# Kernel tuning notes

Measured on AMD Instinct MI355X. Metric: run time of the kernel, lower is better.

The kernel has to match this reference:

```python
import jax, jax.numpy as jnp
import numpy as np

DIM = 768
HEADS = 12
HEAD_DIM = DIM // HEADS
EPS = 1e-5


def setup_inputs() -> dict:
    key = jax.random.key(0)
    ks = jax.random.split(key, 9)
    s = 0.02
    x = jax.random.normal(ks[0], (4, 1024, DIM), dtype=jnp.float32)
    return {
        "x": x,
        "Wqkv_c": jax.random.normal(ks[1], (DIM, 3 * DIM), jnp.float32) * s,
        "bqkv_c": jnp.zeros((3 * DIM,), jnp.float32),
        "Wp_c": jax.random.normal(ks[2], (DIM, DIM), jnp.float32) * s,
        "bp_c": jnp.zeros((DIM,), jnp.float32),
        "Wqkv_ac": jax.random.normal(ks[3], (DIM, 3 * DIM), jnp.float32) * s,
        "bqkv_ac": jnp.zeros((3 * DIM,), jnp.float32),
        "Wp_ac": jax.random.normal(ks[4], (DIM, DIM), jnp.float32) * s,
        "bp_ac": jnp.zeros((DIM,), jnp.float32),
        "gamma": jnp.ones((DIM,), jnp.float32),
        "beta": jnp.zeros((DIM,), jnp.float32),
    }


def _branch(x, Wqkv, bqkv, Wp, bp, causal: bool):
    B, T, C = x.shape
    qkv = (x @ Wqkv + bqkv).reshape(B, T, 3, HEADS, HEAD_DIM)
    qkv = jnp.transpose(qkv, (2, 0, 3, 1, 4))  # [3,B,H,T,Dh]
    q, k, v = qkv[0], qkv[1], qkv[2]
    scores = jnp.einsum("bhqd,bhkd->bhqk", q, k) / np.sqrt(HEAD_DIM).astype(np.float32)
    i = jnp.arange(T)[:, None]
    j = jnp.arange(T)[None, :]
    mask = (j <= i) if causal else (j >= i)  # tril / triu (incl. diagonal)
    scores = jnp.where(mask[None, None], scores, -jnp.inf)
    attn = jax.nn.softmax(scores, axis=-1)
    out = jnp.einsum("bhqk,bhkd->bhqd", attn, v)
    out = jnp.transpose(out, (0, 2, 1, 3)).reshape(B, T, C)
    return out @ Wp + bp


def reference(x, Wqkv_c, bqkv_c, Wp_c, bp_c, Wqkv_ac, bqkv_ac, Wp_ac, bp_ac, gamma, beta):
    out_c = _branch(x, Wqkv_c, bqkv_c, Wp_c, bp_c, causal=True)
    out_ac = _branch(x, Wqkv_ac, bqkv_ac, Wp_ac, bp_ac, causal=False)
    y = x + out_c + out_ac  # residual; dropout is identity at eval
    mu = jnp.mean(y, axis=-1, keepdims=True)
    var = jnp.var(y, axis=-1, keepdims=True)
    return (y - mu) * jax.lax.rsqrt(var + EPS) * gamma + beta
```

## Files before the change

### kernel.cpp

```cpp
#include <hip/hip_runtime.h>
#include <stdint.h>

#define DIM 768
#define HEADS 12
#define HD 64
#define BATCH 4
#define SEQ 1024
#define NTOK (BATCH*SEQ)
#define QKVW (3*DIM)
#define QKW (2*DIM)
#define EPS 1e-5f

typedef __attribute__((ext_vector_type(8))) short short8;
typedef __attribute__((ext_vector_type(4))) float f32x4;

__device__ __forceinline__ unsigned short f2bf(float f) {
    union { float f; unsigned u; } v; v.f = f;
    unsigned r = v.u + 0x7fffu + ((v.u >> 16) & 1u);
    return (unsigned short)(r >> 16);
}
__device__ __forceinline__ float b2f(unsigned short s) {
    union { unsigned u; float f; } v; v.u = (unsigned)s << 16; return v.f;
}

__device__ __forceinline__ void gld_lds16(const void* g, void* l) {
    auto gp = reinterpret_cast<const __attribute__((address_space(1))) unsigned int*>(
        (uintptr_t)g);
    auto lp = reinterpret_cast<__attribute__((address_space(3))) unsigned int*>(
        (unsigned int)(uintptr_t)l);
    __builtin_amdgcn_global_load_lds(gp, lp, 16, 0, 0);
}

#define CVT_X_BLOCKS (NTOK*DIM/4096)
#define CVT_WQ_TILES ((QKVW/32)*(DIM/32))
#define CVT_WP_TILES ((DIM/32)*(DIM/32))
__global__ __launch_bounds__(256) void cvt_all_kernel(
    const float* __restrict__ x,
    const float* __restrict__ Wq0, const float* __restrict__ Wq1,
    const float* __restrict__ Wp0, const float* __restrict__ Wp1,
    unsigned short* __restrict__ xb,
    unsigned short* __restrict__ WqT0, unsigned short* __restrict__ WqT1,
    unsigned short* __restrict__ WpT0, unsigned short* __restrict__ WpT1)
{
    const int bid = blockIdx.x, tid = threadIdx.x;
    if (bid < CVT_X_BLOCKS) {
        const int base = bid * 1024 + tid;
#pragma unroll
        for (int u = 0; u < 4; ++u) {
            const float4 v = ((const float4*)x)[base + u * 256];
            ushort4 o4;
            o4.x = f2bf(v.x); o4.y = f2bf(v.y); o4.z = f2bf(v.z); o4.w = f2bf(v.w);
            ((ushort4*)xb)[base + u * 256] = o4;
        }
        return;
    }
    __shared__ float t[32][33];
    const float* W; unsigned short* WT; int N, K, tile;
    int w = bid - CVT_X_BLOCKS;
    if (w < 2 * CVT_WQ_TILES) {
        const int z = w / CVT_WQ_TILES; tile = w % CVT_WQ_TILES;
        W = z ? Wq1 : Wq0; WT = z ? WqT1 : WqT0; N = QKVW; K = DIM;
    } else {
        w -= 2 * CVT_WQ_TILES;
        const int z = w / CVT_WP_TILES; tile = w % CVT_WP_TILES;
        W = z ? Wp1 : Wp0; WT = z ? WpT1 : WpT0; N = DIM; K = DIM;
    }
    const int ntiles = N / 32;
    const int n0 = (tile % ntiles) * 32, k0 = (tile / ntiles) * 32;
    const int c = tid & 31, rr = tid >> 5;
#pragma unroll
    for (int i = 0; i < 4; ++i)
        t[rr + 8 * i][c] = W[(size_t)(k0 + rr + 8 * i) * N + n0 + c];
    __syncthreads();
#pragma unroll
    for (int i = 0; i < 4; ++i)
        WT[(size_t)(n0 + rr + 8 * i) * K + k0 + c] = f2bf(t[c][rr + 8 * i]);
}

__global__ __launch_bounds__(256) void gemm_qkv_kernel(
    const unsigned short* __restrict__ A,
    const unsigned short* __restrict__ BT0, const unsigned short* __restrict__ BT1,
    const float* __restrict__ bias0, const float* __restrict__ bias1,
    unsigned short* __restrict__ QK0, unsigned short* __restrict__ QK1,
    unsigned short* __restrict__ VT0, unsigned short* __restrict__ VT1)
{
    const int gid = blockIdx.x;
    const int g = gid & 7, t = gid >> 3;
    const int bx = (g & 1) * 9 + t % 9;
    const int by = ((g >> 1) & 1) * 16 + t / 9;
    const int z = g >> 2;
    const unsigned short* __restrict__ BT = z ? BT1 : BT0;
    const float* __restrict__ bias = z ? bias1 : bias0;
    unsigned short* __restrict__ QK = z ? QK1 : QK0;
    unsigned short* __restrict__ VT = z ? VT1 : VT0;
    const int K = DIM;
    const int m0 = by * 128, n0 = bx * 128;

    __shared__ __align__(16) unsigned short sh[17408];
    const int tid = threadIdx.x, lane = tid & 63, wv = tid >> 6;
    const int wr = wv >> 1, wc = wv & 1;
    const int fm = lane & 15, fk = (lane >> 4) * 8;
    const int c0 = wv * 2;
    const int arow = c0 * 16 + (lane >> 2), kk = (lane & 3) * 8;

    const unsigned short* Ag0 = A  + (size_t)(m0 + arow)      * K + kk;
    const unsigned short* Ag1 = A  + (size_t)(m0 + arow + 16) * K + kk;
    const unsigned short* Bg0 = BT + (size_t)(n0 + arow)      * K + kk;
    const unsigned short* Bg1 = BT + (size_t)(n0 + arow + 16) * K + kk;

    f32x4 acc[4][4];
#pragma unroll
    for (int i = 0; i < 4; ++i)
#pragma unroll
        for (int j = 0; j < 4; ++j) acc[i][j] = f32x4{0.f, 0.f, 0.f, 0.f};

    gld_lds16(Ag0, &sh[c0 * 512]);
    gld_lds16(Ag1, &sh[c0 * 512 + 512]);
    gld_lds16(Bg0, &sh[4096 + c0 * 512]);
    gld_lds16(Bg1, &sh[4096 + c0 * 512 + 512]);

    const int NK = K / 32;
    for (int kt = 0; kt < NK; ++kt) {
        const int p = kt & 1;
        __syncthreads();
        if (kt + 1 < NK) {
            const int off = (kt + 1) * 32;
            const int q = (p ^ 1) * 8192;
            gld_lds16(Ag0 + off, &sh[q + c0 * 512]);
            gld_lds16(Ag1 + off, &sh[q + c0 * 512 + 512]);
            gld_lds16(Bg0 + off, &sh[q + 4096 + c0 * 512]);
            gld_lds16(Bg1 + off, &sh[q + 4096 + c0 * 512 + 512]);
        }
        const int pb = p * 8192;
        short8 af[4], bf[4];
#pragma unroll
        for (int i = 0; i < 4; ++i)
            af[i] = *(const short8*)&sh[pb + (wr * 64 + i * 16 + fm) * 32 + fk];
#pragma unroll
        for (int j = 0; j < 4; ++j)
            bf[j] = *(const short8*)&sh[pb + 4096 + (wc * 64 + j * 16 + fm) * 32 + fk];
#pragma unroll
        for (int i = 0; i < 4; ++i)
#pragma unroll
            for (int j = 0; j < 4; ++j)
                acc[i][j] = __builtin_amdgcn_mfma_f32_16x16x32_bf16(af[i], bf[j], acc[i][j], 0, 0, 0);
    }

    __syncthreads();
    const int rbase = (lane >> 4) * 4;
    const int rowg = tid >> 4, lseg = tid & 15;
    if (n0 < QKW) {
        const float qsc = (n0 < DIM) ? 0.125f : 1.0f;
#pragma unroll
        for (int i = 0; i < 4; ++i) {
            const int ml = wr * 64 + i * 16 + rbase;
#pragma unroll
            for (int j = 0; j < 4; ++j) {
                const int nl = wc * 64 + j * 16 + fm;
                const float bs = bias[n0 + nl];
#pragma unroll
                for (int r = 0; r < 4; ++r)
                    sh[(ml + r) * 136 + nl] = f2bf((acc[i][j][r] + bs) * qsc);
            }
        }
        __syncthreads();
#pragma unroll
        for (int pp = 0; pp < 8; ++pp) {
            const int row = pp * 16 + rowg;
            const uint4 v = *(const uint4*)&sh[row * 136 + lseg * 8];
            *(uint4*)(QK + (size_t)(m0 + row) * QKW + n0 + lseg * 8) = v;
        }
    } else {
        const int b = m0 >> 10, t0 = m0 & 1023;
#pragma unroll
        for (int i = 0; i < 4; ++i) {
            const int tl = wr * 64 + i * 16 + rbase;
#pragma unroll
            for (int j = 0; j < 4; ++j) {
                const int nl = wc * 64 + j * 16 + fm;
                const float bs = bias[n0 + nl];
                const unsigned p0 = f2bf(acc[i][j][0] + bs);
                const unsigned p1 = f2bf(acc[i][j][1] + bs);
                const unsigned p2 = f2bf(acc[i][j][2] + bs);
                const unsigned p3 = f2bf(acc[i][j][3] + bs);
                uint2 u; u.x = p0 | (p1 << 16); u.y = p2 | (p3 << 16);
                *(uint2*)(&sh[nl * 136 + tl]) = u;
            }
        }
        __syncthreads();
#pragma unroll
        for (int pp = 0; pp < 8; ++pp) {
            const int nl = pp * 16 + rowg;
            const int nh = (n0 - QKW) + nl;
            const uint4 v = *(const uint4*)&sh[nl * 136 + lseg * 8];
            *(uint4*)(VT + ((size_t)((b * HEADS + (nh >> 6)) * HD + (nh & 63))) * SEQ
                      + t0 + lseg * 8) = v;
        }
    }
}

__global__ __launch_bounds__(256) void gemm_proj_kernel(
    const unsigned short* __restrict__ A0, const unsigned short* __restrict__ BT0,
    const unsigned short* __restrict__ A1, const unsigned short* __restrict__ BT1,
    const float* __restrict__ b0, const float* __restrict__ b1,
    const float* __restrict__ xres, float* __restrict__ Y0,
    unsigned short* __restrict__ Y1)
{
    const int z = blockIdx.z;
    const unsigned short* __restrict__ A  = z ? A1 : A0;
    const unsigned short* __restrict__ BT = z ? BT1 : BT0;
    __shared__ __align__(16) unsigned short Als[2][64 * 32];
    __shared__ __align__(16) unsigned short Bls[2][128 * 32];
    const int tid = threadIdx.x, lane = tid & 63, wv = tid >> 6;
    const int m0 = blockIdx.y * 64, n0 = blockIdx.x * 128;
    const int fm = lane & 15, fg = lane >> 4, fk = (lane >> 4) * 8;
    const int srw = lane >> 2, kk = (lane & 3) * 8;
    const int K = DIM;

    const unsigned short* Ag  = A  + (size_t)(m0 + wv * 16 + srw) * K + kk;
    const unsigned short* Bg0 = BT + (size_t)(n0 + wv * 32 + srw) * K + kk;
    const unsigned short* Bg1 = BT + (size_t)(n0 + wv * 32 + 16 + srw) * K + kk;

    f32x4 acc[4][2];
#pragma unroll
    for (int i = 0; i < 4; ++i)
#pragma unroll
        for (int j = 0; j < 2; ++j) acc[i][j] = f32x4{0.f, 0.f, 0.f, 0.f};

    gld_lds16(Ag,  &Als[0][wv * 512]);
    gld_lds16(Bg0, &Bls[0][wv * 1024]);
    gld_lds16(Bg1, &Bls[0][wv * 1024 + 512]);

    const int NK = K / 32;
    for (int kt = 0; kt < NK; ++kt) {
        const int p = kt & 1;
        __syncthreads();
        if (kt + 1 < NK) {
            const int off = (kt + 1) * 32;
            gld_lds16(Ag + off,  &Als[p ^ 1][wv * 512]);
            gld_lds16(Bg0 + off, &Bls[p ^ 1][wv * 1024]);
            gld_lds16(Bg1 + off, &Bls[p ^ 1][wv * 1024 + 512]);
        }
        short8 af[4], bf[2];
#pragma unroll
        for (int i = 0; i < 4; ++i)
            af[i] = *(const short8*)&Als[p][(i * 16 + fm) * 32 + fk];
#pragma unroll
        for (int j = 0; j < 2; ++j)
            bf[j] = *(const short8*)&Bls[p][(wv * 32 + j * 16 + fm) * 32 + fk];
#pragma unroll
        for (int i = 0; i < 4; ++i)
#pragma unroll
            for (int j = 0; j < 2; ++j)
                acc[i][j] = __builtin_amdgcn_mfma_f32_16x16x32_bf16(af[i], bf[j], acc[i][j], 0, 0, 0);
    }
#pragma unroll
    for (int i = 0; i < 4; ++i) {
        const int m = m0 + i * 16 + fg * 4;
#pragma unroll
        for (int j = 0; j < 2; ++j) {
            const int n = n0 + wv * 32 + j * 16 + fm;
            if (z == 0) {
                const float bs = b0[n] + b1[n];
#pragma unroll
                for (int r = 0; r < 4; ++r) {
                    const size_t idx = (size_t)(m + r) * DIM + n;
                    Y0[idx] = acc[i][j][r] + xres[idx] + bs;
                }
            } else {
#pragma unroll
                for (int r = 0; r < 4; ++r)
                    Y1[(size_t)(m + r) * DIM + n] = f2bf(acc[i][j][r]);
            }
        }
    }
}

#define KP 72
__global__ __launch_bounds__(256, 3) void attn_fused_kernel(
    const unsigned short* __restrict__ qk_c, const unsigned short* __restrict__ vT_c,
    const unsigned short* __restrict__ qk_ac, const unsigned short* __restrict__ vT_ac,
    unsigned short* __restrict__ o_c, unsigned short* __restrict__ o_ac)
{
    __shared__ __align__(16) unsigned short Kls[2][64 * KP];
    __shared__ __align__(16) unsigned short Vls[2][64 * KP];
    __shared__ __align__(16) unsigned short Ps[4][16 * KP];
    const int tid = threadIdx.x, lane = tid & 63, w = tid >> 6;
    const int fm = lane & 15, fg = lane >> 4;
    const int bh = blockIdx.x, qt = blockIdx.y;
    const int b = bh / HEADS, h = bh % HEADS;
    unsigned short* Psw = &Ps[w][0];
    const int srow = tid >> 3, sseg = (tid & 7) * 8;

    for (int br = 0; br < 2; ++br) {
        const int causal = (br == 0);
        const unsigned short* __restrict__ qk = causal ? qk_c : qk_ac;
        const unsigned short* __restrict__ vT = causal ? vT_c : vT_ac;
        unsigned short* __restrict__ o = causal ? o_c : o_ac;
        const unsigned short* qbase = qk + (size_t)b * SEQ * QKW + h * HD;
        const unsigned short* kbase = qbase + DIM;
        const unsigned short* vtb   = vT + (size_t)(b * HEADS + h) * HD * SEQ;

        short8 qb0, qb1;
        {
            const size_t qoff = (size_t)(qt * 64 + w * 16 + fm) * QKW + fg * 8;
            qb0 = *(const short8*)(qbase + qoff);
            qb1 = *(const short8*)(qbase + qoff + 32);
        }

        float ls = 0.f;
        f32x4 accO[4];
#pragma unroll
        for (int dj = 0; dj < 4; ++dj) accO[dj] = f32x4{0.f, 0.f, 0.f, 0.f};

        const int ktb = causal ? 0 : qt;
        const int kte = causal ? qt : (SEQ / 64 - 1);

        uint4 kr0 = *(const uint4*)(kbase + (size_t)(ktb * 64 + srow) * QKW + sseg);
        uint4 kr1 = *(const uint4*)(kbase + (size_t)(ktb * 64 + srow + 32) * QKW + sseg);
        uint4 vr0 = *(const uint4*)(vtb + (size_t)srow * SEQ + ktb * 64 + sseg);
        uint4 vr1 = *(const uint4*)(vtb + (size_t)(srow + 32) * SEQ + ktb * 64 + sseg);

        if (br) __syncthreads();
        int p = 0;
        for (int kt = ktb; kt <= kte; ++kt) {
            *(uint4*)(&Kls[p][srow * KP + sseg])        = kr0;
            *(uint4*)(&Kls[p][(srow + 32) * KP + sseg]) = kr1;
            *(uint4*)(&Vls[p][srow * KP + sseg])        = vr0;
            *(uint4*)(&Vls[p][(srow + 32) * KP + sseg]) = vr1;
            if (kt < kte) {
                const int ktn = kt + 1;
                kr0 = *(const uint4*)(kbase + (size_t)(ktn * 64 + srow) * QKW + sseg);
                kr1 = *(const uint4*)(kbase + (size_t)(ktn * 64 + srow + 32) * QKW + sseg);
                vr0 = *(const uint4*)(vtb + (size_t)srow * SEQ + ktn * 64 + sseg);
                vr1 = *(const uint4*)(vtb + (size_t)(srow + 32) * SEQ + ktn * 64 + sseg);
            }
            __syncthreads();

            f32x4 st[4];
#pragma unroll
            for (int kj = 0; kj < 4; ++kj) {
                const short8 ka0 = *(const short8*)&Kls[p][(kj * 16 + fm) * KP + fg * 8];
                const short8 ka1 = *(const short8*)&Kls[p][(kj * 16 + fm) * KP + 32 + fg * 8];
                st[kj] = __builtin_amdgcn_mfma_f32_16x16x32_bf16(ka0, qb0, f32x4{0.f,0.f,0.f,0.f}, 0, 0, 0);
                st[kj] = __builtin_amdgcn_mfma_f32_16x16x32_bf16(ka1, qb1, st[kj], 0, 0, 0);
            }
            const bool diag = (kt == qt);
#pragma unroll
            for (int kj = 0; kj < 4; ++kj) {
                float e[4];
#pragma unroll
                for (int r = 0; r < 4; ++r) {
                    float v = st[kj][r];
                    if (diag) {
                        const int ki = kj * 16 + fg * 4 + r;
                        const int qi = w * 16 + fm;
                        const bool ok = causal ? (ki <= qi) : (ki >= qi);
                        if (!ok) v = -1e30f;
                    }
                    e[r] = __expf(v);
                    ls += e[r];
                }
                union { float f; unsigned u; } u0, u1, u2, u3;
                u0.f = e[0]; u1.f = e[1]; u2.f = e[2]; u3.f = e[3];
                uint2 u;
                u.x = (u0.u >> 16) | (u1.u & 0xffff0000u);
                u.y = (u2.u >> 16) | (u3.u & 0xffff0000u);
                *(uint2*)(Psw + fm * KP + kj * 16 + fg * 4) = u;
            }
            const short8 ap0 = *(const short8*)(Psw + fm * KP + fg * 8);
            const short8 ap1 = *(const short8*)(Psw + fm * KP + 32 + fg * 8);
#pragma unroll
            for (int dj = 0; dj < 4; ++dj) {
                const short8 vb0 = *(const short8*)&Vls[p][(dj * 16 + fm) * KP + fg * 8];
                const short8 vb1 = *(const short8*)&Vls[p][(dj * 16 + fm) * KP + 32 + fg * 8];
                accO[dj] = __builtin_amdgcn_mfma_f32_16x16x32_bf16(ap0, vb0, accO[dj], 0, 0, 0);
                accO[dj] = __builtin_amdgcn_mfma_f32_16x16x32_bf16(ap1, vb1, accO[dj], 0, 0, 0);
            }
            p ^= 1;
        }

        float lt = ls;
        lt += __shfl_xor(lt, 16);
        lt += __shfl_xor(lt, 32);
        float li_o[4];
#pragma unroll
        for (int r = 0; r < 4; ++r) li_o[r] = __shfl(lt, fg * 4 + r);
#pragma unroll
        for (int r = 0; r < 4; ++r) {
            const float inv = 1.f / li_o[r];
            const int q = qt * 64 + w * 16 + fg * 4 + r;
            unsigned short* orow = o + ((size_t)b * SEQ + q) * DIM + h * HD;
#pragma unroll
            for (int dj = 0; dj < 4; ++dj)
                orow[dj * 16 + fm] = f2bf(accO[dj][r] * inv);
        }
    }
}

__global__ __launch_bounds__(256) void ln_kernel(
    const float* __restrict__ Y0, const unsigned short* __restrict__ Y1,
    const float* __restrict__ gamma, const float* __restrict__ beta,
    float* __restrict__ out)
{
    const int row = blockIdx.x;
    const int tid = threadIdx.x;
    const float* y0r = Y0 + (size_t)row * DIM;
    const unsigned short* y1r = Y1 + (size_t)row * DIM;
    float v0 = y0r[tid]       + b2f(y1r[tid]);
    float v1 = y0r[tid + 256] + b2f(y1r[tid + 256]);
    float v2 = y0r[tid + 512] + b2f(y1r[tid + 512]);
    float s = v0 + v1 + v2;
    float q = v0 * v0 + v1 * v1 + v2 * v2;
#pragma unroll
    for (int off = 32; off > 0; off >>= 1) {
        s += __shfl_down(s, off);
        q += __shfl_down(q, off);
    }
    __shared__ float rs_[4], rq_[4];
    const int wv = tid >> 6;
    if ((tid & 63) == 0) { rs_[wv] = s; rq_[wv] = q; }
    __syncthreads();
    const float ts = rs_[0] + rs_[1] + rs_[2] + rs_[3];
    const float tq = rq_[0] + rq_[1] + rq_[2] + rq_[3];
    const float mu = ts * (1.f / DIM);
    const float var = tq * (1.f / DIM) - mu * mu;
    const float rstd = rsqrtf(var + EPS);
    out[(size_t)row * DIM + tid]       = (v0 - mu) * rstd * gamma[tid]       + beta[tid];
    out[(size_t)row * DIM + tid + 256] = (v1 - mu) * rstd * gamma[tid + 256] + beta[tid + 256];
    out[(size_t)row * DIM + tid + 512] = (v2 - mu) * rstd * gamma[tid + 512] + beta[tid + 512];
}

extern "C" void kernel_launch(void* const* d_in, const int* in_sizes, int n_in,
                              void* d_out, int out_size, void* d_ws, size_t ws_size,
                              hipStream_t stream)
{
    const float* x       = (const float*)d_in[0];
    const float* Wqkv_c  = (const float*)d_in[1];
    const float* bqkv_c  = (const float*)d_in[2];
    const float* Wp_c    = (const float*)d_in[3];
    const float* bp_c    = (const float*)d_in[4];
    const float* Wqkv_ac = (const float*)d_in[5];
    const float* bqkv_ac = (const float*)d_in[6];
    const float* Wp_ac   = (const float*)d_in[7];
    const float* bp_ac   = (const float*)d_in[8];
    const float* gamma   = (const float*)d_in[9];
    const float* beta    = (const float*)d_in[10];
    float* out = (float*)d_out;

    char* p = (char*)d_ws;
    unsigned short* qk_c   = (unsigned short*)p; p += (size_t)NTOK * QKW * 2;
    unsigned short* qk_ac  = (unsigned short*)p; p += (size_t)NTOK * QKW * 2;
    unsigned short* vT_c   = (unsigned short*)p; p += (size_t)NTOK * DIM * 2;
    unsigned short* vT_ac  = (unsigned short*)p; p += (size_t)NTOK * DIM * 2;
    unsigned short* o_ac   = (unsigned short*)p; p += (size_t)NTOK * DIM * 2;
    unsigned short* xb     = (unsigned short*)p; p += (size_t)NTOK * DIM * 2;
    unsigned short* WqT_c  = (unsigned short*)p; p += (size_t)QKVW * DIM * 2;
    unsigned short* WqT_ac = (unsigned short*)p; p += (size_t)QKVW * DIM * 2;
    unsigned short* WpT_c  = (unsigned short*)p; p += (size_t)DIM * DIM * 2;
    unsigned short* WpT_ac = (unsigned short*)p; p += (size_t)DIM * DIM * 2;
    unsigned short* o_c = WqT_c;
    float*          Y0  = (float*)qk_c;
    unsigned short* Y1  = vT_c;

    cvt_all_kernel<<<CVT_X_BLOCKS + 2 * CVT_WQ_TILES + 2 * CVT_WP_TILES, 256, 0, stream>>>(
        x, Wqkv_c, Wqkv_ac, Wp_c, Wp_ac, xb, WqT_c, WqT_ac, WpT_c, WpT_ac);

    gemm_qkv_kernel<<<(QKVW / 128) * (NTOK / 128) * 2, 256, 0, stream>>>(
        xb, WqT_c, WqT_ac, bqkv_c, bqkv_ac, qk_c, qk_ac, vT_c, vT_ac);

    attn_fused_kernel<<<dim3(BATCH * HEADS, SEQ / 64), 256, 0, stream>>>(
        qk_c, vT_c, qk_ac, vT_ac, o_c, o_ac);

    gemm_proj_kernel<<<dim3(DIM / 128, NTOK / 64, 2), 256, 0, stream>>>(
        o_c, WpT_c, o_ac, WpT_ac, bp_c, bp_ac, x, Y0, Y1);
    ln_kernel<<<NTOK, 256, 0, stream>>>(Y0, Y1, gamma, beta, out);
}
```

Baseline: 196.5 us.

## Rewrite QKV GEMM with 256x256 tiles, 8 waves, swizzled LDS and interleaved prefetch

The QKV projection GEMM moves from 128x128 tiles with 4 waves to 256x256 tiles with 8 waves, using a K-step of 64 and an XOR-swizzled LDS layout. Global-to-LDS loads are split into quarters and interleaved between four MFMA phases, with explicit waitcnt, barriers and setprio to overlap memory traffic with compute. The epilogue writes the output in two halves through LDS. The aim is more data reuse per tile and fewer LDS bank conflicts. The cost is a grid of only 288 blocks, higher register pressure from 32 accumulators per thread, and 128 KB of LDS per block.

```diff
diff --git a/kernel.cpp b/kernel.cpp
--- a/kernel.cpp
+++ b/kernel.cpp
@@ -77,7 +77,7 @@
         WT[(size_t)(n0 + rr + 8 * i) * K + k0 + c] = f2bf(t[c][rr + 8 * i]);
 }
 
-__global__ __launch_bounds__(256) void gemm_qkv_kernel(
+__global__ __launch_bounds__(512, 2) void gemm_qkv_kernel(
     const unsigned short* __restrict__ A,
     const unsigned short* __restrict__ BT0, const unsigned short* __restrict__ BT1,
     const float* __restrict__ bias0, const float* __restrict__ bias1,
@@ -85,116 +85,220 @@
     unsigned short* __restrict__ VT0, unsigned short* __restrict__ VT1)
 {
     const int gid = blockIdx.x;
-    const int g = gid & 7, t = gid >> 3;
-    const int bx = (g & 1) * 9 + t % 9;
-    const int by = ((g >> 1) & 1) * 16 + t / 9;
-    const int z = g >> 2;
+    const int wg = (gid & 7) * 36 + (gid >> 3);
+    const int by = wg & 15, bx = wg >> 4;
+    const int z = (bx >= 9) ? 1 : 0;
     const unsigned short* __restrict__ BT = z ? BT1 : BT0;
     const float* __restrict__ bias = z ? bias1 : bias0;
     unsigned short* __restrict__ QK = z ? QK1 : QK0;
     unsigned short* __restrict__ VT = z ? VT1 : VT0;
-    const int K = DIM;
-    const int m0 = by * 128, n0 = bx * 128;
-
-    __shared__ __align__(16) unsigned short sh[17408];
+    const int m0 = by * 256;
+    const int nb0 = (z ? bx - 9 : bx) * 256;
+
+    __shared__ __align__(16) unsigned short lds[65536];
+
     const int tid = threadIdx.x, lane = tid & 63, wv = tid >> 6;
-    const int wr = wv >> 1, wc = wv & 1;
-    const int fm = lane & 15, fk = (lane >> 4) * 8;
-    const int c0 = wv * 2;
-    const int arow = c0 * 16 + (lane >> 2), kk = (lane & 3) * 8;
-
-    const unsigned short* Ag0 = A  + (size_t)(m0 + arow)      * K + kk;
-    const unsigned short* Ag1 = A  + (size_t)(m0 + arow + 16) * K + kk;
-    const unsigned short* Bg0 = BT + (size_t)(n0 + arow)      * K + kk;
-    const unsigned short* Bg1 = BT + (size_t)(n0 + arow + 16) * K + kk;
-
-    f32x4 acc[4][4];
-#pragma unroll
-    for (int i = 0; i < 4; ++i)
+    const int fm = lane & 15, fg = lane >> 4;
+    const int wr = wv >> 2, wc = wv & 3;
+
+    const int sr = lane >> 3;
+    const int sc = ((lane & 7) ^ sr) * 8;
+    const unsigned short* pA = A  + (size_t)(m0  + wv * 16 + sr) * DIM + sc;
+    const unsigned short* pB = BT + (size_t)(nb0 + wv * 16 + sr) * DIM + sc;
+    unsigned short* dA = lds + wv * 1024;
+    unsigned short* dB = lds + 32768 + wv * 1024;
+
+    const int swz = fm & 7;
+    const int cK0 = ((0 + fg) ^ swz) * 8;
+    const int cK1 = ((4 + fg) ^ swz) * 8;
+    const int aB = (wr * 128 + fm) * 64;
+    const int bB = (wc * 64 + fm) * 64;
+
+    f32x4 acc[8][4];
+#pragma unroll
+    for (int i = 0; i < 8; ++i)
 #pragma unroll
         for (int j = 0; j < 4; ++j) acc[i][j] = f32x4{0.f, 0.f, 0.f, 0.f};
 
-    gld_lds16(Ag0, &sh[c0 * 512]);
-    gld_lds16(Ag1, &sh[c0 * 512 + 512]);
-    gld_lds16(Bg0, &sh[4096 + c0 * 512]);
-    gld_lds16(Bg1, &sh[4096 + c0 * 512 + 512]);
-
-    const int NK = K / 32;
-    for (int kt = 0; kt < NK; ++kt) {
-        const int p = kt & 1;
-        __syncthreads();
-        if (kt + 1 < NK) {
-            const int off = (kt + 1) * 32;
-            const int q = (p ^ 1) * 8192;
-            gld_lds16(Ag0 + off, &sh[q + c0 * 512]);
-            gld_lds16(Ag1 + off, &sh[q + c0 * 512 + 512]);
-            gld_lds16(Bg0 + off, &sh[q + 4096 + c0 * 512]);
-            gld_lds16(Bg1 + off, &sh[q + 4096 + c0 * 512 + 512]);
-        }
-        const int pb = p * 8192;
-        short8 af[4], bf[4];
-#pragma unroll
-        for (int i = 0; i < 4; ++i)
-            af[i] = *(const short8*)&sh[pb + (wr * 64 + i * 16 + fm) * 32 + fk];
-#pragma unroll
-        for (int j = 0; j < 4; ++j)
-            bf[j] = *(const short8*)&sh[pb + 4096 + (wc * 64 + j * 16 + fm) * 32 + fk];
-#pragma unroll
-        for (int i = 0; i < 4; ++i)
-#pragma unroll
-            for (int j = 0; j < 4; ++j)
-                acc[i][j] = __builtin_amdgcn_mfma_f32_16x16x32_bf16(af[i], bf[j], acc[i][j], 0, 0, 0);
-    }
-
-    __syncthreads();
-    const int rbase = (lane >> 4) * 4;
-    const int rowg = tid >> 4, lseg = tid & 15;
-    if (n0 < QKW) {
-        const float qsc = (n0 < DIM) ? 0.125f : 1.0f;
-#pragma unroll
-        for (int i = 0; i < 4; ++i) {
-            const int ml = wr * 64 + i * 16 + rbase;
-#pragma unroll
-            for (int j = 0; j < 4; ++j) {
-                const int nl = wc * 64 + j * 16 + fm;
-                const float bs = bias[n0 + nl];
-#pragma unroll
-                for (int r = 0; r < 4; ++r)
-                    sh[(ml + r) * 136 + nl] = f2bf((acc[i][j][r] + bs) * qsc);
-            }
-        }
-        __syncthreads();
-#pragma unroll
-        for (int pp = 0; pp < 8; ++pp) {
-            const int row = pp * 16 + rowg;
-            const uint4 v = *(const uint4*)&sh[row * 136 + lseg * 8];
-            *(uint4*)(QK + (size_t)(m0 + row) * QKW + n0 + lseg * 8) = v;
+    short8 a[4][2], b0[2][2], b1[2][2];
+
+    gld_lds16(pA,             dA);
+    gld_lds16(pA + 8 * DIM,   dA + 512);
+    gld_lds16(pA + 128 * DIM, dA + 8192);
+    gld_lds16(pA + 136 * DIM, dA + 8192 + 512);
+    gld_lds16(pB,             dB);
+    gld_lds16(pB + 8 * DIM,   dB + 512);
+    gld_lds16(pB + 128 * DIM, dB + 8192);
+    gld_lds16(pB + 136 * DIM, dB + 8192 + 512);
+
+    for (int t = 0; t < 12; ++t) {
+        const int ab = (t & 1) * 16384;
+        const int bb = 32768 + (t & 1) * 16384;
+        const int nb = ((t + 1) & 1) * 16384;
+        const int kN = (t + 1) * 64;
+        const bool more = (t < 11);
+
+        if (more) {
+            gld_lds16(pA + kN,           dA + nb);
+            gld_lds16(pA + kN + 8 * DIM, dA + nb + 512);
+            asm volatile("s_waitcnt vmcnt(2)" ::: "memory");
+        } else {
+            asm volatile("s_waitcnt vmcnt(0)" ::: "memory");
+        }
+        __builtin_amdgcn_s_barrier();
+#pragma unroll
+        for (int mi = 0; mi < 4; ++mi) {
+            a[mi][0] = *(const short8*)&lds[ab + aB + mi * 1024 + cK0];
+            a[mi][1] = *(const short8*)&lds[ab + aB + mi * 1024 + cK1];
+        }
+#pragma unroll
+        for (int nj = 0; nj < 2; ++nj) {
+            b0[nj][0] = *(const short8*)&lds[bb + bB + nj * 1024 + cK0];
+            b0[nj][1] = *(const short8*)&lds[bb + bB + nj * 1024 + cK1];
+        }
+        asm volatile("s_waitcnt lgkmcnt(0)" ::: "memory");
+        __builtin_amdgcn_sched_barrier(0);
+        __builtin_amdgcn_s_setprio(1);
+#pragma unroll
+        for (int ks = 0; ks < 2; ++ks)
+#pragma unroll
+            for (int mi = 0; mi < 4; ++mi)
+#pragma unroll
+                for (int nj = 0; nj < 2; ++nj)
+                    acc[mi][nj] = __builtin_amdgcn_mfma_f32_16x16x32_bf16(
+                        a[mi][ks], b0[nj][ks], acc[mi][nj], 0, 0, 0);
+        __builtin_amdgcn_s_setprio(0);
+        __builtin_amdgcn_s_barrier();
+
+#pragma unroll
+        for (int nj = 0; nj < 2; ++nj) {
+            b1[nj][0] = *(const short8*)&lds[bb + bB + 2048 + nj * 1024 + cK0];
+            b1[nj][1] = *(const short8*)&lds[bb + bB + 2048 + nj * 1024 + cK1];
+        }
+        if (more) {
+            gld_lds16(pA + kN + 128 * DIM, dA + nb + 8192);
+            gld_lds16(pA + kN + 136 * DIM, dA + nb + 8192 + 512);
+        }
+        __builtin_amdgcn_s_barrier();
+        asm volatile("s_waitcnt lgkmcnt(0)" ::: "memory");
+        __builtin_amdgcn_sched_barrier(0);
+        __builtin_amdgcn_s_setprio(1);
+#pragma unroll
+        for (int ks = 0; ks < 2; ++ks)
+#pragma unroll
+            for (int mi = 0; mi < 4; ++mi)
+#pragma unroll
+                for (int nj = 0; nj < 2; ++nj)
+                    acc[mi][2 + nj] = __builtin_amdgcn_mfma_f32_16x16x32_bf16(
+                        a[mi][ks], b1[nj][ks], acc[mi][2 + nj], 0, 0, 0);
+        __builtin_amdgcn_s_setprio(0);
+        __builtin_amdgcn_s_barrier();
+
+#pragma unroll
+        for (int mi = 0; mi < 4; ++mi) {
+            a[mi][0] = *(const short8*)&lds[ab + aB + 4096 + mi * 1024 + cK0];
+            a[mi][1] = *(const short8*)&lds[ab + aB + 4096 + mi * 1024 + cK1];
+        }
+        if (more) {
+            gld_lds16(pB + kN,           dB + nb);
+            gld_lds16(pB + kN + 8 * DIM, dB + nb + 512);
+        }
+        __builtin_amdgcn_s_barrier();
+        asm volatile("s_waitcnt lgkmcnt(0)" ::: "memory");
+        __builtin_amdgcn_sched_barrier(0);
+        __builtin_amdgcn_s_setprio(1);
+#pragma unroll
+        for (int ks = 0; ks < 2; ++ks)
+#pragma unroll
+            for (int mi = 0; mi < 4; ++mi)
+#pragma unroll
+                for (int nj = 0; nj < 2; ++nj)
+                    acc[4 + mi][2 + nj] = __builtin_amdgcn_mfma_f32_16x16x32_bf16(
+                        a[mi][ks], b1[nj][ks], acc[4 + mi][2 + nj], 0, 0, 0);
+        __builtin_amdgcn_s_setprio(0);
+        __builtin_amdgcn_s_barrier();
+
+        if (more) {
+            gld_lds16(pB + kN + 128 * DIM, dB + nb + 8192);
+            gld_lds16(pB + kN + 136 * DIM, dB + nb + 8192 + 512);
+        }
+        __builtin_amdgcn_s_barrier();
+        asm volatile("s_waitcnt lgkmcnt(0)" ::: "memory");
+        __builtin_amdgcn_sched_barrier(0);
+        __builtin_amdgcn_s_setprio(1);
+#pragma unroll
+        for (int ks = 0; ks < 2; ++ks)
+#pragma unroll
+            for (int mi = 0; mi < 4; ++mi)
+#pragma unroll
+                for (int nj = 0; nj < 2; ++nj)
+                    acc[4 + mi][nj] = __builtin_amdgcn_mfma_f32_16x16x32_bf16(
+                        a[mi][ks], b0[nj][ks], acc[4 + mi][nj], 0, 0, 0);
+        __builtin_amdgcn_s_setprio(0);
+        __builtin_amdgcn_s_barrier();
+    }
+
+    if (nb0 < QKW) {
+        const float qsc = (nb0 < DIM) ? 0.125f : 1.0f;
+#pragma unroll
+        for (int h = 0; h < 2; ++h) {
+            __syncthreads();
+            if (wr == h) {
+#pragma unroll
+                for (int ai = 0; ai < 8; ++ai) {
+#pragma unroll
+                    for (int bj = 0; bj < 4; ++bj) {
+                        const int col = wc * 64 + bj * 16 + fm;
+                        const float bs = bias[nb0 + col];
+#pragma unroll
+                        for (int r = 0; r < 4; ++r) {
+                            const int rl = ai * 16 + fg * 4 + r;
+                            lds[rl * 264 + col] = f2bf((acc[ai][bj][r] + bs) * qsc);
+                        }
+                    }
+                }
+            }
+            __syncthreads();
+#pragma unroll
+            for (int pass = 0; pass < 8; ++pass) {
+                const int row = pass * 16 + (tid >> 5);
+                const int ch = tid & 31;
+                const uint4 v = *(const uint4*)&lds[row * 264 + ch * 8];
+                *(uint4*)(QK + (size_t)(m0 + h * 128 + row) * QKW + nb0 + ch * 8) = v;
+            }
         }
     } else {
         const int b = m0 >> 10, t0 = m0 & 1023;
 #pragma unroll
-        for (int i = 0; i < 4; ++i) {
-            const int tl = wr * 64 + i * 16 + rbase;
-#pragma unroll
-            for (int j = 0; j < 4; ++j) {
-                const int nl = wc * 64 + j * 16 + fm;
-                const float bs = bias[n0 + nl];
-                const unsigned p0 = f2bf(acc[i][j][0] + bs);
-                const unsigned p1 = f2bf(acc[i][j][1] + bs);
-                const unsigned p2 = f2bf(acc[i][j][2] + bs);
-                const unsigned p3 = f2bf(acc[i][j][3] + bs);
-                uint2 u; u.x = p0 | (p1 << 16); u.y = p2 | (p3 << 16);
-                *(uint2*)(&sh[nl * 136 + tl]) = u;
-            }
-        }
-        __syncthreads();
-#pragma unroll
-        for (int pp = 0; pp < 8; ++pp) {
-            const int nl = pp * 16 + rowg;
-            const int nh = (n0 - QKW) + nl;
-            const uint4 v = *(const uint4*)&sh[nl * 136 + lseg * 8];
-            *(uint4*)(VT + ((size_t)((b * HEADS + (nh >> 6)) * HD + (nh & 63))) * SEQ
-                      + t0 + lseg * 8) = v;
+        for (int h = 0; h < 2; ++h) {
+            __syncthreads();
+            if (wr == h) {
+#pragma unroll
+                for (int ai = 0; ai < 8; ++ai) {
+                    const int tl = ai * 16 + fg * 4;
+#pragma unroll
+                    for (int bj = 0; bj < 4; ++bj) {
+                        const int d = wc * 64 + bj * 16 + fm;
+                        const float bs = bias[nb0 + d];
+                        const unsigned p0 = f2bf(acc[ai][bj][0] + bs);
+                        const unsigned p1 = f2bf(acc[ai][bj][1] + bs);
+                        const unsigned p2 = f2bf(acc[ai][bj][2] + bs);
+                        const unsigned p3 = f2bf(acc[ai][bj][3] + bs);
+                        uint2 u; u.x = p0 | (p1 << 16); u.y = p2 | (p3 << 16);
+                        *(uint2*)&lds[d * 136 + tl] = u;
+                    }
+                }
+            }
+            __syncthreads();
+#pragma unroll
+            for (int pass = 0; pass < 8; ++pass) {
+                const int d = pass * 32 + (tid >> 4);
+                const int tc = tid & 15;
+                const uint4 v = *(const uint4*)&lds[d * 136 + tc * 8];
+                const int dg = nb0 - QKW + d;
+                *(uint4*)(VT + ((size_t)((b * HEADS + (dg >> 6)) * HD + (dg & 63))) * SEQ
+                          + t0 + h * 128 + tc * 8) = v;
+            }
         }
     }
 }
@@ -466,7 +570,7 @@
     cvt_all_kernel<<<CVT_X_BLOCKS + 2 * CVT_WQ_TILES + 2 * CVT_WP_TILES, 256, 0, stream>>>(
         x, Wqkv_c, Wqkv_ac, Wp_c, Wp_ac, xb, WqT_c, WqT_ac, WpT_c, WpT_ac);
 
-    gemm_qkv_kernel<<<(QKVW / 128) * (NTOK / 128) * 2, 256, 0, stream>>>(
+    gemm_qkv_kernel<<<288, 512, 0, stream>>>(
         xb, WqT_c, WqT_ac, bqkv_c, bqkv_ac, qk_c, qk_ac, vT_c, vT_ac);
 
     attn_fused_kernel<<<dim3(BATCH * HEADS, SEQ / 64), 256, 0, stream>>>(
```

After: 203.2 us. +3.4%, slower.

## Rework QKV GEMM with BK=64 swizzled LDS tiles and XCD-aware block mapping

Applied to the files above, without the earlier changes.

Rewrites the QKV projection GEMM main loop to use 64-wide K tiles (12 iterations instead of 24) with an XOR-swizzled LDS layout to avoid bank conflicts. The MFMA work is split into two half-phases with explicit waitcnt/sched_barrier and setprio hints. Block IDs are remapped so each group of 8 consecutive IDs (likely one per XCD) covers contiguous M rows. LDS grows to 64KB, and launch bounds request 2 blocks per CU, which may constrain registers.

```diff
diff --git a/kernel.cpp b/kernel.cpp
--- a/kernel.cpp
+++ b/kernel.cpp
@@ -77,7 +77,7 @@
         WT[(size_t)(n0 + rr + 8 * i) * K + k0 + c] = f2bf(t[c][rr + 8 * i]);
 }
 
-__global__ __launch_bounds__(256) void gemm_qkv_kernel(
+__global__ __launch_bounds__(256, 2) void gemm_qkv_kernel(
     const unsigned short* __restrict__ A,
     const unsigned short* __restrict__ BT0, const unsigned short* __restrict__ BT1,
     const float* __restrict__ bias0, const float* __restrict__ bias1,
@@ -85,28 +85,36 @@
     unsigned short* __restrict__ VT0, unsigned short* __restrict__ VT1)
 {
     const int gid = blockIdx.x;
-    const int g = gid & 7, t = gid >> 3;
-    const int bx = (g & 1) * 9 + t % 9;
-    const int by = ((g >> 1) & 1) * 16 + t / 9;
-    const int z = g >> 2;
+    const int wg = (gid & 7) * 144 + (gid >> 3);
+    const int by = wg & 31;
+    const int bxz = wg >> 5;
+    const int z = (bxz >= 18) ? 1 : 0;
+    const int bx = z ? bxz - 18 : bxz;
     const unsigned short* __restrict__ BT = z ? BT1 : BT0;
     const float* __restrict__ bias = z ? bias1 : bias0;
     unsigned short* __restrict__ QK = z ? QK1 : QK0;
     unsigned short* __restrict__ VT = z ? VT1 : VT0;
-    const int K = DIM;
-    const int m0 = by * 128, n0 = bx * 128;
-
-    __shared__ __align__(16) unsigned short sh[17408];
+    const int m0 = by * 128;
+    const int nb0 = bx * 128;
+
+    __shared__ __align__(16) unsigned short lds[32768];
+
     const int tid = threadIdx.x, lane = tid & 63, wv = tid >> 6;
+    const int fm = lane & 15, fg = lane >> 4;
     const int wr = wv >> 1, wc = wv & 1;
-    const int fm = lane & 15, fk = (lane >> 4) * 8;
-    const int c0 = wv * 2;
-    const int arow = c0 * 16 + (lane >> 2), kk = (lane & 3) * 8;
-
-    const unsigned short* Ag0 = A  + (size_t)(m0 + arow)      * K + kk;
-    const unsigned short* Ag1 = A  + (size_t)(m0 + arow + 16) * K + kk;
-    const unsigned short* Bg0 = BT + (size_t)(n0 + arow)      * K + kk;
-    const unsigned short* Bg1 = BT + (size_t)(n0 + arow + 16) * K + kk;
+
+    const int sr8 = lane >> 3;
+    const int sc = ((lane & 7) ^ sr8) * 8;
+    const unsigned short* pA = A  + (size_t)(m0  + wv * 8 + sr8) * DIM + sc;
+    const unsigned short* pB = BT + (size_t)(nb0 + wv * 8 + sr8) * DIM + sc;
+    unsigned short* dA = lds + wv * 512;
+    unsigned short* dB = lds + 16384 + wv * 512;
+
+    const int swz = fm & 7;
+    const int cK0 = ((0 + fg) ^ swz) * 8;
+    const int cK1 = ((4 + fg) ^ swz) * 8;
+    const int aB = (wr * 64 + fm) * 64;
+    const int bB = (wc * 64 + fm) * 64;
 
     f32x4 acc[4][4];
 #pragma unroll
@@ -114,86 +122,120 @@
 #pragma unroll
         for (int j = 0; j < 4; ++j) acc[i][j] = f32x4{0.f, 0.f, 0.f, 0.f};
 
-    gld_lds16(Ag0, &sh[c0 * 512]);
-    gld_lds16(Ag1, &sh[c0 * 512 + 512]);
-    gld_lds16(Bg0, &sh[4096 + c0 * 512]);
-    gld_lds16(Bg1, &sh[4096 + c0 * 512 + 512]);
-
-    const int NK = K / 32;
-    for (int kt = 0; kt < NK; ++kt) {
-        const int p = kt & 1;
-        __syncthreads();
-        if (kt + 1 < NK) {
-            const int off = (kt + 1) * 32;
-            const int q = (p ^ 1) * 8192;
-            gld_lds16(Ag0 + off, &sh[q + c0 * 512]);
-            gld_lds16(Ag1 + off, &sh[q + c0 * 512 + 512]);
-            gld_lds16(Bg0 + off, &sh[q + 4096 + c0 * 512]);
-            gld_lds16(Bg1 + off, &sh[q + 4096 + c0 * 512 + 512]);
-        }
-        const int pb = p * 8192;
-        short8 af[4], bf[4];
-#pragma unroll
-        for (int i = 0; i < 4; ++i)
-            af[i] = *(const short8*)&sh[pb + (wr * 64 + i * 16 + fm) * 32 + fk];
-#pragma unroll
-        for (int j = 0; j < 4; ++j)
-            bf[j] = *(const short8*)&sh[pb + 4096 + (wc * 64 + j * 16 + fm) * 32 + fk];
-#pragma unroll
-        for (int i = 0; i < 4; ++i)
-#pragma unroll
-            for (int j = 0; j < 4; ++j)
-                acc[i][j] = __builtin_amdgcn_mfma_f32_16x16x32_bf16(af[i], bf[j], acc[i][j], 0, 0, 0);
+    short8 a[4][2], b[4][2];
+
+#pragma unroll
+    for (int j = 0; j < 4; ++j) {
+        gld_lds16(pA + j * 32 * DIM, dA + j * 2048);
+        gld_lds16(pB + j * 32 * DIM, dB + j * 2048);
+    }
+
+    for (int t = 0; t < 12; ++t) {
+        const int ab = (t & 1) * 8192;
+        const int bb = 16384 + (t & 1) * 8192;
+        const int nb2 = ((t + 1) & 1) * 8192;
+
+        asm volatile("s_waitcnt vmcnt(0)" ::: "memory");
+        __builtin_amdgcn_s_barrier();
+        if (t < 11) {
+            const int kN = (t + 1) * 64;
+#pragma unroll
+            for (int j = 0; j < 4; ++j) {
+                gld_lds16(pA + kN + j * 32 * DIM, dA + nb2 + j * 2048);
+                gld_lds16(pB + kN + j * 32 * DIM, dB + nb2 + j * 2048);
+            }
+        }
+
+#pragma unroll
+        for (int mi = 0; mi < 4; ++mi) {
+            a[mi][0] = *(const short8*)&lds[ab + aB + mi * 1024 + cK0];
+            a[mi][1] = *(const short8*)&lds[ab + aB + mi * 1024 + cK1];
+        }
+#pragma unroll
+        for (int nj = 0; nj < 2; ++nj) {
+            b[nj][0] = *(const short8*)&lds[bb + bB + nj * 1024 + cK0];
+            b[nj][1] = *(const short8*)&lds[bb + bB + nj * 1024 + cK1];
+        }
+        asm volatile("s_waitcnt lgkmcnt(0)" ::: "memory");
+        __builtin_amdgcn_sched_barrier(0);
+        __builtin_amdgcn_s_setprio(1);
+#pragma unroll
+        for (int ks = 0; ks < 2; ++ks)
+#pragma unroll
+            for (int mi = 0; mi < 4; ++mi)
+#pragma unroll
+                for (int nj = 0; nj < 2; ++nj)
+                    acc[mi][nj] = __builtin_amdgcn_mfma_f32_16x16x32_bf16(
+                        a[mi][ks], b[nj][ks], acc[mi][nj], 0, 0, 0);
+        __builtin_amdgcn_s_setprio(0);
+
+#pragma unroll
+        for (int nj = 2; nj < 4; ++nj) {
+            b[nj][0] = *(const short8*)&lds[bb + bB + nj * 1024 + cK0];
+            b[nj][1] = *(const short8*)&lds[bb + bB + nj * 1024 + cK1];
+        }
+        asm volatile("s_waitcnt lgkmcnt(0)" ::: "memory");
+        __builtin_amdgcn_sched_barrier(0);
+        __builtin_amdgcn_s_setprio(1);
+#pragma unroll
+        for (int ks = 0; ks < 2; ++ks)
+#pragma unroll
+            for (int mi = 0; mi < 4; ++mi)
+#pragma unroll
+                for (int nj = 2; nj < 4; ++nj)
+                    acc[mi][nj] = __builtin_amdgcn_mfma_f32_16x16x32_bf16(
+                        a[mi][ks], b[nj][ks], acc[mi][nj], 0, 0, 0);
+        __builtin_amdgcn_s_setprio(0);
     }
 
     __syncthreads();
-    const int rbase = (lane >> 4) * 4;
+    const int rbase = fg * 4;
     const int rowg = tid >> 4, lseg = tid & 15;
-    if (n0 < QKW) {
-        const float qsc = (n0 < DIM) ? 0.125f : 1.0f;
+    if (nb0 < QKW) {
+        const float qsc = (nb0 < DIM) ? 0.125f : 1.0f;
 #pragma unroll
         for (int i = 0; i < 4; ++i) {
             const int ml = wr * 64 + i * 16 + rbase;
 #pragma unroll
             for (int j = 0; j < 4; ++j) {
                 const int nl = wc * 64 + j * 16 + fm;
-                const float bs = bias[n0 + nl];
+                const float bs = bias[nb0 + nl];
 #pragma unroll
                 for (int r = 0; r < 4; ++r)
-                    sh[(ml + r) * 136 + nl] = f2bf((acc[i][j][r] + bs) * qsc);
+                    lds[(ml + r) * 136 + nl] = f2bf((acc[i][j][r] + bs) * qsc);
             }
         }
         __syncthreads();
 #pragma unroll
         for (int pp = 0; pp < 8; ++pp) {
             const int row = pp * 16 + rowg;
-            const uint4 v = *(const uint4*)&sh[row * 136 + lseg * 8];
-            *(uint4*)(QK + (size_t)(m0 + row) * QKW + n0 + lseg * 8) = v;
+            const uint4 v = *(const uint4*)&lds[row * 136 + lseg * 8];
+            *(uint4*)(QK + (size_t)(m0 + row) * QKW + nb0 + lseg * 8) = v;
         }
     } else {
-        const int b = m0 >> 10, t0 = m0 & 1023;
+        const int b8 = m0 >> 10, t0 = m0 & 1023;
 #pragma unroll
         for (int i = 0; i < 4; ++i) {
             const int tl = wr * 64 + i * 16 + rbase;
 #pragma unroll
             for (int j = 0; j < 4; ++j) {
                 const int nl = wc * 64 + j * 16 + fm;
-                const float bs = bias[n0 + nl];
+                const float bs = bias[nb0 + nl];
                 const unsigned p0 = f2bf(acc[i][j][0] + bs);
                 const unsigned p1 = f2bf(acc[i][j][1] + bs);
                 const unsigned p2 = f2bf(acc[i][j][2] + bs);
                 const unsigned p3 = f2bf(acc[i][j][3] + bs);
                 uint2 u; u.x = p0 | (p1 << 16); u.y = p2 | (p3 << 16);
-                *(uint2*)(&sh[nl * 136 + tl]) = u;
+                *(uint2*)(&lds[nl * 136 + tl]) = u;
             }
         }
         __syncthreads();
 #pragma unroll
         for (int pp = 0; pp < 8; ++pp) {
             const int nl = pp * 16 + rowg;
-            const int nh = (n0 - QKW) + nl;
-            const uint4 v = *(const uint4*)&sh[nl * 136 + lseg * 8];
-            *(uint4*)(VT + ((size_t)((b * HEADS + (nh >> 6)) * HD + (nh & 63))) * SEQ
+            const int nh = (nb0 - QKW) + nl;
+            const uint4 v = *(const uint4*)&lds[nl * 136 + lseg * 8];
+            *(uint4*)(VT + ((size_t)((b8 * HEADS + (nh >> 6)) * HD + (nh & 63))) * SEQ
                       + t0 + lseg * 8) = v;
         }
     }
@@ -466,7 +508,7 @@
     cvt_all_kernel<<<CVT_X_BLOCKS + 2 * CVT_WQ_TILES + 2 * CVT_WP_TILES, 256, 0, stream>>>(
         x, Wqkv_c, Wqkv_ac, Wp_c, Wp_ac, xb, WqT_c, WqT_ac, WpT_c, WpT_ac);
 
-    gemm_qkv_kernel<<<(QKVW / 128) * (NTOK / 128) * 2, 256, 0, stream>>>(
+    gemm_qkv_kernel<<<1152, 256, 0, stream>>>(
         xb, WqT_c, WqT_ac, bqkv_c, bqkv_ac, qk_c, qk_ac, vT_c, vT_ac);
 
     attn_fused_kernel<<<dim3(BATCH * HEADS, SEQ / 64), 256, 0, stream>>>(
```

Result: no change. 197.1 us (+0.3%).
